# Performance work log

Measured on AMD Instinct MI355X. Metric: run time of the kernel, lower is better.

Reference implementation:

```python
import jax, jax.numpy as jnp
import numpy as np

R = 4
SCALING = 2.0  # lora_alpha / r = 2r/r
NUM_EXPERTS = 3
TOP_K = 1
EPS = 1e-6
C = 64
DW = 128   # c * DW_Expand
FFN = 128  # c * FFN_Expand
B, H, W = 4, 256, 256
K3 = 3


def _conv(x, w, groups, pad):
    return jax.lax.conv_general_dilated(
        x, w, (1, 1), [(pad, pad), (pad, pad)],
        dimension_numbers=('NCHW', 'OIHW', 'NCHW'),
        feature_group_count=groups)


def conv2dmix(x, w, b, la, lb, gate, groups, pad):
    # base conv + top-k gated mixture of LoRA expert deltas (conv is linear in w)
    out = _conv(x, w, groups, pad) + b[None, :, None, None]
    for e in range(NUM_EXPERTS):
        dw = (lb[e] @ la[e]).reshape(w.shape) * SCALING  # low-rank delta weight
        out = out + gate[:, e][:, None, None, None] * _conv(x, dw, groups, pad)
    return out


def ln2d(x, w, b):
    mu = jnp.mean(x, axis=1, keepdims=True)
    var = jnp.var(x, axis=1, keepdims=True)
    return (x - mu) / jnp.sqrt(var + EPS) * w[None, :, None, None] + b[None, :, None, None]


def simple_gate(x):
    x1, x2 = jnp.split(x, 2, axis=1)
    return x1 * x2


def setup_inputs() -> dict:
    key = jax.random.key(0)
    ks = list(jax.random.split(key, 40))
    k = iter(ks)
    rn = lambda shape, s=0.05: jax.random.normal(next(k), shape, dtype=jnp.float32) * s
    d = {}
    d['inp'] = jax.random.normal(next(k), (B, C, H, W), dtype=jnp.float32)
    d['probs'] = jax.random.uniform(next(k), (B, NUM_EXPERTS), dtype=jnp.float32)
    d['ln1_w'] = jnp.ones((C,), jnp.float32); d['ln1_b'] = jnp.zeros((C,), jnp.float32)
    d['ln2_w'] = jnp.ones((C,), jnp.float32); d['ln2_b'] = jnp.zeros((C,), jnp.float32)
    # conv1: 1x1, C -> DW
    d['w1'] = rn((DW, C, 1, 1)); d['b1'] = jnp.zeros((DW,), jnp.float32)
    d['la1'] = rn((NUM_EXPERTS, R, C)); d['lb1'] = rn((NUM_EXPERTS, DW, R))
    # conv2: 3x3 depthwise, DW -> DW, groups=DW  (loralib ConvLoRA shapes)
    d['w2'] = rn((DW, 1, K3, K3)); d['b2'] = jnp.zeros((DW,), jnp.float32)
    d['la2'] = rn((NUM_EXPERTS, R * K3, 1 * K3)); d['lb2'] = rn((NUM_EXPERTS, DW * K3, R * K3))
    # sca conv: 1x1, DW//2 -> DW//2
    d['wsca'] = rn((DW // 2, DW // 2, 1, 1)); d['bsca'] = jnp.zeros((DW // 2,), jnp.float32)
    d['lasca'] = rn((NUM_EXPERTS, R, DW // 2)); d['lbsca'] = rn((NUM_EXPERTS, DW // 2, R))
    # conv3: 1x1, DW//2 -> C
    d['w3'] = rn((C, DW // 2, 1, 1)); d['b3'] = jnp.zeros((C,), jnp.float32)
    d['la3'] = rn((NUM_EXPERTS, R, DW // 2)); d['lb3'] = rn((NUM_EXPERTS, C, R))
    # conv4: 1x1, C -> FFN
    d['w4'] = rn((FFN, C, 1, 1)); d['b4'] = jnp.zeros((FFN,), jnp.float32)
    d['la4'] = rn((NUM_EXPERTS, R, C)); d['lb4'] = rn((NUM_EXPERTS, FFN, R))
    # conv5: 1x1, FFN//2 -> C
    d['w5'] = rn((C, FFN // 2, 1, 1)); d['b5'] = jnp.zeros((C,), jnp.float32)
    d['la5'] = rn((NUM_EXPERTS, R, FFN // 2)); d['lb5'] = rn((NUM_EXPERTS, C, R))
    d['beta'] = jnp.zeros((1, C, 1, 1), jnp.float32) + 0.1
    d['gamma'] = jnp.zeros((1, C, 1, 1), jnp.float32) + 0.1
    return d


def reference(inp, probs, ln1_w, ln1_b, ln2_w, ln2_b,
              w1, b1, la1, lb1, w2, b2, la2, lb2,
              wsca, bsca, lasca, lbsca, w3, b3, la3, lb3,
              w4, b4, la4, lb4, w5, b5, la5, lb5, beta, gamma):
    # top-k gate per sample: keep top_k probs, zero the rest (no renorm)
    vals, idx = jax.lax.top_k(probs, TOP_K)
    gate = jnp.zeros_like(probs).at[jnp.arange(probs.shape[0])[:, None], idx].set(vals)

    x = ln2d(inp, ln1_w, ln1_b)
    x = conv2dmix(x, w1, b1, la1, lb1, gate, 1, 0)
    x = conv2dmix(x, w2, b2, la2, lb2, gate, DW, 1)
    x = simple_gate(x)
    pooled = jnp.mean(x, axis=(2, 3), keepdims=True)
    x = x * conv2dmix(pooled, wsca, bsca, lasca, lbsca, gate, 1, 0)
    x = conv2dmix(x, w3, b3, la3, lb3, gate, 1, 0)
    y = inp + x * beta
    x = conv2dmix(ln2d(y, ln2_w, ln2_b), w4, b4, la4, lb4, gate, 1, 0)
    x = simple_gate(x)
    x = conv2dmix(x, w5, b5, la5, lb5, gate, 1, 0)
    return y + x * gamma
```

## Files before the change

kernel.cpp:

```cpp
#include <hip/hip_runtime.h>
#include <hip/hip_bf16.h>

#define HW 65536
#define WST 29952

typedef unsigned short U16;
typedef __attribute__((ext_vector_type(8))) short short8;
typedef __attribute__((ext_vector_type(4))) unsigned short us4;
typedef __attribute__((ext_vector_type(4))) float float4v;

#define WEFF_OFF 0
#define FRAG_OFF 524288
#define POOL_OFF 786432
#define SCA_OFF  787456
#define Z_OFF    68157440

__device__ inline U16 f2bf(float f) {
  union { float f; unsigned u; } v; v.f = f;
  unsigned r = v.u + 0x7FFF + ((v.u >> 16) & 1);
  return (U16)(r >> 16);
}
__device__ inline unsigned pack2(float a, float b) {
  union { __hip_bfloat162 h; unsigned u; } v;
  v.h = __float22bfloat162_rn(float2{a, b});
  return v.u;
}
__device__ inline float bf2f(U16 h) {
  union { unsigned u; float f; } v; v.u = ((unsigned)h) << 16;
  return v.f;
}
__device__ inline float asfhi(unsigned u) {
  union { unsigned u; float f; } v; v.u = u & 0xffff0000u; return v.f;
}
__device__ inline float asflo(unsigned u) {
  union { unsigned u; float f; } v; v.u = u << 16; return v.f;
}

__global__ __launch_bounds__(256) void k_weights(const float* __restrict__ probs,
    const float* __restrict__ w1, const float* __restrict__ la1, const float* __restrict__ lb1,
    const float* __restrict__ w2, const float* __restrict__ la2, const float* __restrict__ lb2,
    const float* __restrict__ wsca, const float* __restrict__ lasca, const float* __restrict__ lbsca,
    const float* __restrict__ w3, const float* __restrict__ la3, const float* __restrict__ lb3,
    const float* __restrict__ w4, const float* __restrict__ la4, const float* __restrict__ lb4,
    const float* __restrict__ w5, const float* __restrict__ la5, const float* __restrict__ lb5,
    const float* __restrict__ b3, const float* __restrict__ b5,
    const float* __restrict__ beta, const float* __restrict__ gamma,
    const float* __restrict__ ln1w, const float* __restrict__ ln1b, const float* __restrict__ b1,
    float* __restrict__ weff, U16* __restrict__ fragw)
{
  __shared__ float sb[5952];
  int blk = blockIdx.x;
  int b = blk / 6, sec = blk - b * 6;
  int tid = threadIdx.x;
  float p0 = probs[b*3+0], p1 = probs[b*3+1], p2 = probs[b*3+2];
  int e = 0; float g = p0;
  if (p1 > g) { g = p1; e = 1; }
  if (p2 > g) { g = p2; e = 2; }
  float s = 2.0f * g;
  float* wfp = weff + b * WST;
  U16* fws = fragw + b * 24576;

  if (sec == 1) {
    const float* lbs = lb2 + e * 4608;
    const float* las = la2 + e * 36;
    for (int i = tid; i < 4608; i += 256) sb[i] = lbs[i];
    if (tid < 36) sb[4608 + tid] = las[tid];
    if (tid < 64) {
      sb[4644 + tid] = b3[tid];  sb[4708 + tid] = b5[tid];
      sb[4772 + tid] = beta[tid]; sb[4836 + tid] = gamma[tid];
      sb[5668 + tid] = ln1w[tid]; sb[5732 + tid] = ln1b[tid];
    }
    if (tid < 256) sb[4900 + tid] = la1[e*256 + tid];
    for (int i = tid; i < 512; i += 256) sb[5156 + i] = lb1[e*512 + i];
    if (tid < 128) sb[5796 + tid] = b1[tid];
    __syncthreads();
    for (int idx = tid; idx < 1152; idx += 256) {
      int row = idx / 3, dx = idx - row * 3;
      float acc = w2[idx];
      #pragma unroll
      for (int r = 0; r < 12; ++r)
        acc += s * sb[row*12 + r] * sb[4608 + r*3 + dx];
      wfp[8192 + idx] = acc;
    }
    if (tid < 64) {
      wfp[29824 + tid] = sb[4644 + tid] * sb[4772 + tid];
      wfp[29888 + tid] = sb[4708 + tid] * sb[4836 + tid];
    }
    if (tid >= 128) {
      int n = tid - 128;
      float S = 0.f, Bn = sb[5796 + n];
      for (int c = 0; c < 64; ++c) {
        float wv = w1[n*64 + c];
        #pragma unroll
        for (int r = 0; r < 4; ++r) wv += s * sb[5156 + n*4 + r] * sb[4900 + r*64 + c];
        S  += bf2f(f2bf(wv * sb[5668 + c]));
        Bn += wv * sb[5732 + c];
      }
      wfp[n] = S; wfp[128 + n] = Bn;
    }
    return;
  }
  if (sec == 2) {
    const float* lbs = lbsca + e * 256;
    const float* las = lasca + e * 256;
    if (tid < 256) { sb[tid] = lbs[tid]; sb[256 + tid] = las[tid]; }
    __syncthreads();
    #pragma unroll 4
    for (int idx = tid; idx < 4096; idx += 256) {
      int c = idx >> 6, k = idx & 63;
      float acc = wsca[k*64 + c];
      #pragma unroll
      for (int r = 0; r < 4; ++r)
        acc += s * sb[k*4 + r] * sb[256 + r*64 + c];
      wfp[9344 + idx] = acc;
    }
    return;
  }

  const float *w, *la, *lb, *scl = nullptr;
  bool sclk = false;
  int fo, cnt;
  if (sec == 0)      { w = w1; lb = lb1 + e*512; la = la1 + e*256; fo = 0;     cnt = 8192; scl = ln1w; sclk = true; }
  else if (sec == 3) { w = w3; lb = lb3 + e*256; la = la3 + e*256; fo = 8192;  cnt = 4096; scl = beta; }
  else if (sec == 4) { w = w4; lb = lb4 + e*512; la = la4 + e*256; fo = 12288; cnt = 8192; }
  else               { w = w5; lb = lb5 + e*256; la = la5 + e*256; fo = 20480; cnt = 4096; scl = gamma; }
  int nlb = (cnt == 8192) ? 512 : 256;
  for (int i = tid; i < nlb; i += 256) sb[i] = lb[i];
  if (tid < 256) sb[512 + tid] = la[tid];
  if (scl && tid < 64) sb[768 + tid] = scl[tid];
  __syncthreads();
  #pragma unroll 4
  for (int idx = tid; idx < cnt; idx += 256) {
    int j = idx & 7, l = (idx >> 3) & 63, s2 = (idx >> 9) & 1, nt = idx >> 10;
    int n = nt*16 + (l & 15), k = s2*32 + ((l >> 4) << 3) + j;
    float acc = w[n*64 + k];
    #pragma unroll
    for (int r = 0; r < 4; ++r)
      acc += s * sb[n*4 + r] * sb[512 + r*64 + k];
    if (scl) acc *= sb[768 + (sclk ? k : n)];
    fws[fo + idx] = f2bf(acc);
  }
}

#define MTS 22
__global__ __launch_bounds__(256, 3) void k_stage1f(
    const float* __restrict__ inp, const float* __restrict__ b2,
    const float* __restrict__ weff, const U16* __restrict__ fragw,
    U16* __restrict__ z, float* __restrict__ pooled)
{
  __shared__ __align__(16) U16 smu[22528];
  __shared__ float2 muinv[344];
  __shared__ float poolbuf[4][16];
  int blk = blockIdx.x;
  int tile = blk & 255;
  int g = (blk >> 8) & 1;
  int b = blk >> 9;
  int h0 = (tile >> 3) * 8, w0 = (tile & 7) * 32;
  int tid = threadIdx.x, lane = tid & 63, w = tid >> 6;
  const float* wfp = weff + b * WST;
  const U16* fw = fragw + b * 24576;

  for (int it = 0; it < 2; ++it) {
    int i = tid + it * 256;
    if (i >= 340) break;
    int hy = i / 34, hx = i - hy * 34;
    int h = h0 - 1 + hy, ww = w0 - 1 + hx;
    int mt = i >> 4, m = i & 15;
    if (h >= 0 && h < 256 && ww >= 0 && ww < 256) {
      const float* src = inp + (size_t)b * 64 * HW + h * 256 + ww;
      float x[64];
      #pragma unroll
      for (int c = 0; c < 64; ++c) x[c] = src[(size_t)c * HW];
      float s0=0,s1=0,q0=0,q1=0;
      #pragma unroll
      for (int c = 0; c < 64; c += 2) {
        s0 += x[c];   q0 += x[c]*x[c];
        s1 += x[c+1]; q1 += x[c+1]*x[c+1];
      }
      float mu  = (s0+s1) * (1.f/64.f);
      float inv = rsqrtf(fmaxf((q0+q1)*(1.f/64.f) - mu*mu, 0.f) + 1e-6f);
      muinv[i] = float2{mu, inv};
      #pragma unroll
      for (int s = 0; s < 2; ++s)
        #pragma unroll
        for (int q = 0; q < 4; ++q) {
          union { unsigned u[4]; short8 v; } pk;
          #pragma unroll
          for (int j = 0; j < 4; ++j)
            pk.u[j] = pack2(x[s*32 + q*8 + 2*j], x[s*32 + q*8 + 2*j + 1]);
          *(short8*)&smu[mt*1024 + s*512 + (q*16 + m)*8] = pk.v;
        }
    } else {
      muinv[i] = float2{0.f, 0.f};
    }
  }

  int n15 = lane & 15;
  short8 bw[8];
  float Sr[4], Br[4];
  #pragma unroll
  for (int ntl = 0; ntl < 4; ++ntl) {
    int ntg = (ntl < 2) ? (g*2 + ntl) : (4 + g*2 + (ntl - 2));
    #pragma unroll
    for (int s = 0; s < 2; ++s)
      bw[ntl*2 + s] = *(const short8*)&fw[((ntg*2 + s)*64 + lane)*8];
    int ng = ntg*16 + n15;
    Sr[ntl] = wfp[ng];
    Br[ntl] = wfp[128 + ng];
  }
  __syncthreads();

  int mt0 = w * 6;
  int nmt = MTS - mt0; if (nmt > 6) nmt = 6;
  float4v acc[6][4];
  #pragma unroll
  for (int mi = 0; mi < 6; ++mi)
    #pragma unroll
    for (int ntl = 0; ntl < 4; ++ntl) acc[mi][ntl] = (float4v)(0.f);
  #pragma unroll
  for (int mi = 0; mi < 6; ++mi) {
    if (mi < nmt) {
      int mt = mt0 + mi;
      #pragma unroll
      for (int s = 0; s < 2; ++s) {
        short8 a = *(const short8*)&smu[mt*1024 + s*512 + lane*8];
        #pragma unroll
        for (int ntl = 0; ntl < 4; ++ntl)
          acc[mi][ntl] = __builtin_amdgcn_mfma_f32_16x16x32_bf16(a, bw[ntl*2 + s], acc[mi][ntl], 0, 0, 0);
      }
    }
  }
  __syncthreads();

  int q = lane >> 4;
  #pragma unroll
  for (int mi = 0; mi < 6; ++mi) {
    if (mi < nmt) {
      int px0 = (mt0 + mi)*16 + q*4;
      if (px0 < 340) {
        float2 m0 = muinv[px0], m1 = muinv[px0+1], m2 = muinv[px0+2], m3 = muinv[px0+3];
        #pragma unroll
        for (int ntl = 0; ntl < 4; ++ntl) {
          float S = Sr[ntl], B = Br[ntl];
          float v0 = m0.y*(acc[mi][ntl][0] - m0.x*S) + B;
          float v1 = m1.y*(acc[mi][ntl][1] - m1.x*S) + B;
          float v2 = m2.y*(acc[mi][ntl][2] - m2.x*S) + B;
          float v3 = m3.y*(acc[mi][ntl][3] - m3.x*S) + B;
          v0 = m0.y > 0.f ? v0 : 0.f;
          v1 = m1.y > 0.f ? v1 : 0.f;
          v2 = m2.y > 0.f ? v2 : 0.f;
          v3 = m3.y > 0.f ? v3 : 0.f;
          union { unsigned u[2]; us4 v; } pk;
          pk.u[0] = pack2(v0, v1);
          pk.u[1] = pack2(v2, v3);
          *(us4*)&smu[(ntl*16 + n15)*348 + px0] = pk.v;
        }
      }
    }
  }
  __syncthreads();

  {
    int half = tid >> 7;
    int pp = (tid & 127) * 2;
    int cy = pp >> 5, cx = pp & 31;
    const float* w2e = wfp + 8192;
    U16* zb = z + (size_t)b*64*HW + (size_t)(h0 + cy)*256 + (w0 + cx);
    #pragma unroll 2
    for (int i = 0; i < 16; ++i) {
      int kl = half*16 + i;
      int kg = g*32 + kl;
      unsigned ua[3][2], uc[3][2];
      #pragma unroll
      for (int dy = 0; dy < 3; ++dy) {
        int basea = kl*348 + (cy + dy)*34 + cx;
        int basec = (32 + kl)*348 + (cy + dy)*34 + cx;
        ua[dy][0] = *(unsigned*)&smu[basea]; ua[dy][1] = *(unsigned*)&smu[basea + 2];
        uc[dy][0] = *(unsigned*)&smu[basec]; uc[dy][1] = *(unsigned*)&smu[basec + 2];
      }
      const float* wa = w2e + kg*9;
      const float* wc = w2e + (kg + 64)*9;
      float a0 = b2[kg], a1 = a0;
      float c0 = b2[kg + 64], c1 = c0;
      #pragma unroll
      for (int dy = 0; dy < 3; ++dy) {
        float x0 = asflo(ua[dy][0]), x1 = asfhi(ua[dy][0]), x2 = asflo(ua[dy][1]), x3 = asfhi(ua[dy][1]);
        a0 += wa[dy*3]*x0 + wa[dy*3+1]*x1 + wa[dy*3+2]*x2;
        a1 += wa[dy*3]*x1 + wa[dy*3+1]*x2 + wa[dy*3+2]*x3;
        x0 = asflo(uc[dy][0]); x1 = asfhi(uc[dy][0]); x2 = asflo(uc[dy][1]); x3 = asfhi(uc[dy][1]);
        c0 += wc[dy*3]*x0 + wc[dy*3+1]*x1 + wc[dy*3+2]*x2;
        c1 += wc[dy*3]*x1 + wc[dy*3+1]*x2 + wc[dy*3+2]*x3;
      }
      float z0 = a0*c0, z1 = a1*c1;
      *(unsigned*)(zb + (size_t)kg * HW) = pack2(z0, z1);
      float ps = z0 + z1;
      #pragma unroll
      for (int off = 32; off >= 1; off >>= 1) ps += __shfl_down(ps, off, 64);
      if (lane == 0) poolbuf[w][i] = ps;
    }
  }
  __syncthreads();
  if (tid < 32) {
    float v = (tid < 16) ? (poolbuf[0][tid] + poolbuf[1][tid])
                         : (poolbuf[2][tid - 16] + poolbuf[3][tid - 16]);
    atomicAdd(&pooled[b*64 + g*32 + tid], v);
  }
}

__global__ void k_sca(const float* __restrict__ bsca, const float* __restrict__ weff,
                      const float* __restrict__ pooled, float* __restrict__ sca)
{
  int b = blockIdx.x, k = threadIdx.x;
  const float* wt = weff + b * WST + 9344;
  const float* pm = pooled + b * 64;
  float acc = bsca[k];
  for (int c = 0; c < 64; ++c) acc += wt[c * 64 + k] * (pm[c] * (1.f/65536.f));
  sca[b * 64 + k] = acc;
}

__global__ __launch_bounds__(256, 2) void k_stage2(
    const float* __restrict__ inp, const U16* __restrict__ z, const float* __restrict__ sca,
    const float* __restrict__ ln2w, const float* __restrict__ ln2b, const float* __restrict__ b4,
    const float* __restrict__ weff, const U16* __restrict__ fragw, float* __restrict__ out)
{
  __shared__ __align__(16) U16 yb[256*72];
  __shared__ __align__(16) char afr[34816];
  U16* afrag = (U16*)afr;
  float* afragF = (float*)afr;
  int blk = blockIdx.x;
  int b = blk >> 8, h = blk & 255;
  int tid = threadIdx.x, lane = tid & 63, w = tid >> 6;
  const float* wb = weff + b * WST;
  const U16* fw = fragw + b * 24576;

  float y0[64];
  {
    const U16* zp = z + (size_t)b*64*HW + h*256 + tid;
    const float* scb = sca + b*64;
    float xs[64];
    #pragma unroll
    for (int k = 0; k < 64; ++k) xs[k] = bf2f(zp[(size_t)k * HW]) * scb[k];
    int mt = tid >> 4, m = tid & 15;
    #pragma unroll
    for (int s = 0; s < 2; ++s)
      #pragma unroll
      for (int q = 0; q < 4; ++q) {
        union { unsigned u[4]; short8 v; } pk;
        #pragma unroll
        for (int j = 0; j < 4; ++j)
          pk.u[j] = pack2(xs[s*32 + q*8 + 2*j], xs[s*32 + q*8 + 2*j + 1]);
        *(short8*)&afrag[mt*1024 + s*512 + (q*16 + m)*8] = pk.v;
      }
    const float* ip = inp + (size_t)b*64*HW + h*256 + tid;
    #pragma unroll
    for (int c = 0; c < 64; ++c) y0[c] = ip[(size_t)c * HW];
  }
  __syncthreads();

  {
    short8 bw3[8];
    #pragma unroll
    for (int i = 0; i < 8; ++i) bw3[i] = *(const short8*)&fw[8192 + (i*64 + lane)*8];
    float4v acc[4][4];
    #pragma unroll
    for (int mi = 0; mi < 4; ++mi)
      #pragma unroll
      for (int nt = 0; nt < 4; ++nt) acc[mi][nt] = (float4v)(0.f);
    #pragma unroll
    for (int mi = 0; mi < 4; ++mi) {
      int mt = w*4 + mi;
      #pragma unroll
      for (int s = 0; s < 2; ++s) {
        short8 a = *(const short8*)&afrag[mt*1024 + s*512 + lane*8];
        #pragma unroll
        for (int nt = 0; nt < 4; ++nt)
          acc[mi][nt] = __builtin_amdgcn_mfma_f32_16x16x32_bf16(a, bw3[nt*2 + s], acc[mi][nt], 0, 0, 0);
      }
    }
    #pragma unroll
    for (int mi = 0; mi < 4; ++mi) {
      int pxb = (w*4 + mi)*16 + ((lane >> 4) << 2);
      #pragma unroll
      for (int nt = 0; nt < 4; ++nt) {
        int c = nt*16 + (lane & 15);
        #pragma unroll
        for (int r = 0; r < 4; ++r)
          yb[(pxb + r)*72 + c] = f2bf(acc[mi][nt][r]);
      }
    }
  }
  __syncthreads();

  {
    const float* b3b = wb + 29824;
    float y[64];
    #pragma unroll
    for (int c8 = 0; c8 < 8; ++c8) {
      short8 v = *(const short8*)&yb[tid*72 + c8*8];
      #pragma unroll
      for (int j = 0; j < 8; ++j) y[c8*8 + j] = bf2f((U16)v[j]);
    }
    #pragma unroll
    for (int c = 0; c < 64; ++c) y[c] += y0[c] + b3b[c];
    float s0=0,s1=0,q0=0,q1=0;
    #pragma unroll
    for (int c = 0; c < 64; c += 2) {
      s0 += y[c];   q0 += y[c]*y[c];
      s1 += y[c+1]; q1 += y[c+1]*y[c+1];
    }
    float mu  = (s0+s1) * (1.f/64.f);
    float inv = rsqrtf((q0+q1) * (1.f/64.f) - mu*mu + 1e-6f);
    int mt = tid >> 4, m = tid & 15;
    #pragma unroll
    for (int s = 0; s < 2; ++s)
      #pragma unroll
      for (int q = 0; q < 4; ++q) {
        union { unsigned u[4]; short8 v; } pk;
        #pragma unroll
        for (int j = 0; j < 4; ++j) {
          int c = s*32 + q*8 + 2*j;
          float e0 = (y[c]   - mu) * inv * ln2w[c]   + ln2b[c];
          float e1 = (y[c+1] - mu) * inv * ln2w[c+1] + ln2b[c+1];
          pk.u[j] = pack2(e0, e1);
        }
        *(short8*)&afrag[mt*1024 + s*512 + (q*16 + m)*8] = pk.v;
      }
    #pragma unroll
    for (int c8 = 0; c8 < 8; ++c8) {
      union { unsigned u[4]; short8 v; } pk;
      #pragma unroll
      for (int j = 0; j < 4; ++j)
        pk.u[j] = pack2(y[c8*8 + 2*j], y[c8*8 + 2*j + 1]);
      *(short8*)&yb[tid*72 + c8*8] = pk.v;
    }
  }
  __syncthreads();

  float4v acc5[4][4];
  {
    short8 bw4[16];
    #pragma unroll
    for (int i = 0; i < 16; ++i) bw4[i] = *(const short8*)&fw[12288 + (i*64 + lane)*8];
    float b4a[8];
    #pragma unroll
    for (int nt = 0; nt < 8; ++nt) b4a[nt] = b4[nt*16 + (lane & 15)];
    float4v acc[4][8];
    #pragma unroll
    for (int mi = 0; mi < 4; ++mi)
      #pragma unroll
      for (int nt = 0; nt < 8; ++nt) acc[mi][nt] = (float4v)(0.f);
    #pragma unroll
    for (int mi = 0; mi < 4; ++mi) {
      int mt = w*4 + mi;
      #pragma unroll
      for (int s = 0; s < 2; ++s) {
        short8 a = *(const short8*)&afrag[mt*1024 + s*512 + lane*8];
        #pragma unroll
        for (int nt = 0; nt < 8; ++nt)
          acc[mi][nt] = __builtin_amdgcn_mfma_f32_16x16x32_bf16(a, bw4[nt*2 + s], acc[mi][nt], 0, 0, 0);
      }
    }
    #pragma unroll
    for (int mi = 0; mi < 4; ++mi) {
      int mt = w*4 + mi;
      int mloc = ((lane >> 4) << 2);
      #pragma unroll
      for (int nt = 0; nt < 4; ++nt) {
        int k = nt*16 + (lane & 15);
        int s_ = k >> 5, q = (k >> 3) & 3, j = k & 7;
        #pragma unroll
        for (int r = 0; r < 4; ++r) {
          float gv = (acc[mi][nt][r] + b4a[nt]) * (acc[mi][nt+4][r] + b4a[nt+4]);
          afrag[mt*1024 + s_*512 + (q*16 + mloc + r)*8 + j] = f2bf(gv);
        }
      }
    }
    short8 bw5[8];
    #pragma unroll
    for (int i = 0; i < 8; ++i) bw5[i] = *(const short8*)&fw[20480 + (i*64 + lane)*8];
    #pragma unroll
    for (int mi = 0; mi < 4; ++mi)
      #pragma unroll
      for (int nt = 0; nt < 4; ++nt) acc5[mi][nt] = (float4v)(0.f);
    #pragma unroll
    for (int mi = 0; mi < 4; ++mi) {
      int mt = w*4 + mi;
      #pragma unroll
      for (int s = 0; s < 2; ++s) {
        short8 a = *(const short8*)&afrag[mt*1024 + s*512 + lane*8];
        #pragma unroll
        for (int nt = 0; nt < 4; ++nt)
          acc5[mi][nt] = __builtin_amdgcn_mfma_f32_16x16x32_bf16(a, bw5[nt*2 + s], acc5[mi][nt], 0, 0, 0);
      }
    }
  }
  __syncthreads();

  {
    const float* b5g = wb + 29888;
    float b5f[4];
    #pragma unroll
    for (int nt = 0; nt < 4; ++nt) b5f[nt] = b5g[nt*16 + (lane & 15)];
    float* op = out + (size_t)b*64*HW + h*256;
    for (int chalf = 0; chalf < 2; ++chalf) {
      #pragma unroll
      for (int mi = 0; mi < 4; ++mi) {
        int pxb = (w*4 + mi)*16 + ((lane >> 4) << 2);
        #pragma unroll
        for (int nt2 = 0; nt2 < 2; ++nt2) {
          int nt = chalf*2 + nt2;
          int c = nt*16 + (lane & 15);
          #pragma unroll
          for (int r = 0; r < 4; ++r) {
            float v = acc5[mi][nt][r] + b5f[nt] + bf2f(yb[(pxb + r)*72 + c]);
            afragF[(pxb + r)*33 + (c - chalf*32)] = v;
          }
        }
      }
      #pragma unroll 4
      for (int cc = 0; cc < 32; ++cc)
        op[(size_t)(chalf*32 + cc) * HW + tid] = afragF[tid*33 + cc];
    }
  }
}

extern "C" void kernel_launch(void* const* d_in, const int* in_sizes, int n_in,
                              void* d_out, int out_size, void* d_ws, size_t ws_size,
                              hipStream_t stream) {
  const float* inp   = (const float*)d_in[0];
  const float* probs = (const float*)d_in[1];
  const float* ln1w  = (const float*)d_in[2];
  const float* ln1b  = (const float*)d_in[3];
  const float* ln2w  = (const float*)d_in[4];
  const float* ln2b  = (const float*)d_in[5];
  const float* w1    = (const float*)d_in[6];
  const float* b1    = (const float*)d_in[7];
  const float* la1   = (const float*)d_in[8];
  const float* lb1   = (const float*)d_in[9];
  const float* w2    = (const float*)d_in[10];
  const float* b2    = (const float*)d_in[11];
  const float* la2   = (const float*)d_in[12];
  const float* lb2   = (const float*)d_in[13];
  const float* wsca  = (const float*)d_in[14];
  const float* bsca  = (const float*)d_in[15];
  const float* lasca = (const float*)d_in[16];
  const float* lbsca = (const float*)d_in[17];
  const float* w3    = (const float*)d_in[18];
  const float* b3    = (const float*)d_in[19];
  const float* la3   = (const float*)d_in[20];
  const float* lb3   = (const float*)d_in[21];
  const float* w4    = (const float*)d_in[22];
  const float* b4    = (const float*)d_in[23];
  const float* la4   = (const float*)d_in[24];
  const float* lb4   = (const float*)d_in[25];
  const float* w5    = (const float*)d_in[26];
  const float* b5    = (const float*)d_in[27];
  const float* la5   = (const float*)d_in[28];
  const float* lb5   = (const float*)d_in[29];
  const float* beta  = (const float*)d_in[30];
  const float* gamma = (const float*)d_in[31];

  char* wsb = (char*)d_ws;
  float* weff   = (float*)(wsb + WEFF_OFF);
  U16*   fragw  = (U16*)(wsb + FRAG_OFF);
  float* pooled = (float*)(wsb + POOL_OFF);
  float* scap   = (float*)(wsb + SCA_OFF);
  U16*   zws    = (U16*)(wsb + Z_OFF);
  float* outp   = (float*)d_out;

  hipMemsetAsync(pooled, 0, 256 * sizeof(float), stream);
  k_weights<<<dim3(24), dim3(256), 0, stream>>>(probs,
      w1, la1, lb1, w2, la2, lb2, wsca, lasca, lbsca,
      w3, la3, lb3, w4, la4, lb4, w5, la5, lb5,
      b3, b5, beta, gamma, ln1w, ln1b, b1, weff, fragw);
  k_stage1f<<<dim3(2048), dim3(256), 0, stream>>>(inp, b2, weff, fragw, zws, pooled);
  k_sca<<<dim3(4), dim3(64), 0, stream>>>(bsca, weff, pooled, scap);
  k_stage2<<<dim3(1024), dim3(256), 0, stream>>>(inp, zws, scap, ln2w, ln2b, b4, weff, fragw, outp);
}
```

Measured before the change: 288.5 us.

## Fuse SCA kernel into stage2 and replace per-channel shuffle pooling with LDS transpose reduce

The tiny k_sca launch is removed. Each stage2 block now recomputes the 64-wide SCA vector from the pooled sums and the effective weights into shared memory before use. In stage1f, the per-channel 64-lane shuffle reductions in the depthwise loop are replaced by per-thread partial sums, followed by one shared-memory transpose and a short tree reduction before the atomics. This trades one kernel launch and many shuffles for redundant per-block SCA work and extra syncs and registers, since the inner loop is now fully unrolled with 16 partial sums.

After: 303.5 us. 5.2% more time.

```diff
diff --git a/kernel.cpp b/kernel.cpp
--- a/kernel.cpp
+++ b/kernel.cpp
@@ -150,7 +150,6 @@
 {
   __shared__ __align__(16) U16 smu[22528];
   __shared__ float2 muinv[344];
-  __shared__ float poolbuf[4][16];
   int blk = blockIdx.x;
   int tile = blk & 255;
   int g = (blk >> 8) & 1;
@@ -260,13 +259,14 @@
   }
   __syncthreads();
 
+  float psum[16];
   {
     int half = tid >> 7;
     int pp = (tid & 127) * 2;
     int cy = pp >> 5, cx = pp & 31;
     const float* w2e = wfp + 8192;
     U16* zb = z + (size_t)b*64*HW + (size_t)(h0 + cy)*256 + (w0 + cx);
-    #pragma unroll 2
+    #pragma unroll
     for (int i = 0; i < 16; ++i) {
       int kl = half*16 + i;
       int kg = g*32 + kl;
@@ -293,38 +293,38 @@
       }
       float z0 = a0*c0, z1 = a1*c1;
       *(unsigned*)(zb + (size_t)kg * HW) = pack2(z0, z1);
-      float ps = z0 + z1;
-      #pragma unroll
-      for (int off = 32; off >= 1; off >>= 1) ps += __shfl_down(ps, off, 64);
-      if (lane == 0) poolbuf[w][i] = ps;
-    }
-  }
-  __syncthreads();
-  if (tid < 32) {
-    float v = (tid < 16) ? (poolbuf[0][tid] + poolbuf[1][tid])
-                         : (poolbuf[2][tid - 16] + poolbuf[3][tid - 16]);
-    atomicAdd(&pooled[b*64 + g*32 + tid], v);
-  }
-}
-
-__global__ void k_sca(const float* __restrict__ bsca, const float* __restrict__ weff,
-                      const float* __restrict__ pooled, float* __restrict__ sca)
-{
-  int b = blockIdx.x, k = threadIdx.x;
-  const float* wt = weff + b * WST + 9344;
-  const float* pm = pooled + b * 64;
-  float acc = bsca[k];
-  for (int c = 0; c < 64; ++c) acc += wt[c * 64 + k] * (pm[c] * (1.f/65536.f));
-  sca[b * 64 + k] = acc;
+      psum[i] = z0 + z1;
+    }
+  }
+  __syncthreads();
+  {
+    float* fs = (float*)smu;
+    #pragma unroll
+    for (int i = 0; i < 16; ++i) fs[tid*17 + i] = psum[i];
+    __syncthreads();
+    int ch = tid >> 3, sub = tid & 7;
+    int hf = ch >> 4, ii = ch & 15;
+    float v = 0.f;
+    #pragma unroll
+    for (int j = 0; j < 16; ++j)
+      v += fs[(hf*128 + sub*16 + j)*17 + ii];
+    v += __shfl_down(v, 4, 64);
+    v += __shfl_down(v, 2, 64);
+    v += __shfl_down(v, 1, 64);
+    if (sub == 0) atomicAdd(&pooled[b*64 + g*32 + ch], v);
+  }
 }
 
 __global__ __launch_bounds__(256, 2) void k_stage2(
-    const float* __restrict__ inp, const U16* __restrict__ z, const float* __restrict__ sca,
+    const float* __restrict__ inp, const U16* __restrict__ z,
+    const float* __restrict__ bsca, const float* __restrict__ pooled,
     const float* __restrict__ ln2w, const float* __restrict__ ln2b, const float* __restrict__ b4,
     const float* __restrict__ weff, const U16* __restrict__ fragw, float* __restrict__ out)
 {
   __shared__ __align__(16) U16 yb[256*72];
   __shared__ __align__(16) char afr[34816];
+  __shared__ float spart[256];
+  __shared__ float ssca[64];
   U16* afrag = (U16*)afr;
   float* afragF = (float*)afr;
   int blk = blockIdx.x;
@@ -333,13 +333,29 @@
   const float* wb = weff + b * WST;
   const U16* fw = fragw + b * 24576;
 
+  {
+    int k = tid & 63, qq = tid >> 6;
+    const float* wt = wb + 9344;
+    const float* pm = pooled + b * 64;
+    float part = 0.f;
+    #pragma unroll
+    for (int j = 0; j < 16; ++j) {
+      int c = qq * 16 + j;
+      part += wt[c * 64 + k] * (pm[c] * (1.f/65536.f));
+    }
+    spart[tid] = part;
+  }
+  __syncthreads();
+  if (tid < 64)
+    ssca[tid] = bsca[tid] + spart[tid] + spart[64 + tid] + spart[128 + tid] + spart[192 + tid];
+  __syncthreads();
+
   float y0[64];
   {
     const U16* zp = z + (size_t)b*64*HW + h*256 + tid;
-    const float* scb = sca + b*64;
     float xs[64];
     #pragma unroll
-    for (int k = 0; k < 64; ++k) xs[k] = bf2f(zp[(size_t)k * HW]) * scb[k];
+    for (int k = 0; k < 64; ++k) xs[k] = bf2f(zp[(size_t)k * HW]) * ssca[k];
     int mt = tid >> 4, m = tid & 15;
     #pragma unroll
     for (int s = 0; s < 2; ++s)
@@ -564,7 +580,6 @@
   float* weff   = (float*)(wsb + WEFF_OFF);
   U16*   fragw  = (U16*)(wsb + FRAG_OFF);
   float* pooled = (float*)(wsb + POOL_OFF);
-  float* scap   = (float*)(wsb + SCA_OFF);
   U16*   zws    = (U16*)(wsb + Z_OFF);
   float* outp   = (float*)d_out;
 
@@ -574,6 +589,5 @@
       w3, la3, lb3, w4, la4, lb4, w5, la5, lb5,
       b3, b5, beta, gamma, ln1w, ln1b, b1, weff, fragw);
   k_stage1f<<<dim3(2048), dim3(256), 0, stream>>>(inp, b2, weff, fragw, zws, pooled);
-  k_sca<<<dim3(4), dim3(64), 0, stream>>>(bsca, weff, pooled, scap);
-  k_stage2<<<dim3(1024), dim3(256), 0, stream>>>(inp, zws, scap, ln2w, ln2b, b4, weff, fragw, outp);
-}
+  k_stage2<<<dim3(1024), dim3(256), 0, stream>>>(inp, zws, bsca, pooled, ln2w, ln2b, b4, weff, fragw, outp);
+}
```
